# Optimization experiments

Hardware: AMD Instinct MI355X
Metric: run time of the kernel (lower is better)

Reference implementation:

```python
import jax, jax.numpy as jnp
import numpy as np

B, N, H = 4, 4096, 64
T1 = 3072  # num_types = [0, 3072, 1024]


def _xavier(key, shape):
    fan_in, fan_out = shape[1], shape[0]
    lim = float(np.sqrt(6.0 / (fan_in + fan_out)))
    return jax.random.uniform(key, shape, jnp.float32, -lim, lim)


def setup_inputs() -> dict:
    key = jax.random.key(0)
    ks = jax.random.split(key, 16)
    adjacency = (jax.random.uniform(ks[0], (N, N)) < 0.05).astype(jnp.float32)
    adjacency = jnp.maximum(adjacency, jnp.eye(N, dtype=jnp.float32))  # avoid all-zero rows
    return {
        "hidden_states": jax.random.normal(ks[1], (B, N, H), jnp.float32),
        "input_states": jax.random.normal(ks[2], (B, 1, 1), jnp.float32),
        "adjacency": adjacency,
        "Wq": _xavier(ks[3], (H, H)),
        "Wk": _xavier(ks[4], (H, H)),
        "Wv": _xavier(ks[5], (H, H)),
        "Wu_inter": _xavier(ks[6], (H, H)),
        "bu_inter": jnp.zeros((H,), jnp.float32),
        "Wt_inter": _xavier(ks[7], (H, H)),
        "bt_inter": jnp.zeros((H,), jnp.float32),
        "Wu_out": _xavier(ks[8], (H, H)),
        "bu_out": jnp.zeros((H,), jnp.float32),
        "Wt_out": _xavier(ks[9], (H, H)),
        "bt_out": jnp.zeros((H,), jnp.float32),
        "step_size": jnp.float32(0.01),
    }


def reference(hidden_states, input_states, adjacency, Wq, Wk, Wv,
              Wu_inter, bu_inter, Wt_inter, bt_inter,
              Wu_out, bu_out, Wt_out, bt_out, step_size):
    # AccumulatorFunction: adjacency-masked QK^T, L2-norm rows (NOT softmax), aggregate V
    mask = adjacency.T  # [N, N]
    q = hidden_states @ Wq.T  # [B, N, H]
    k = hidden_states @ Wk.T
    v = hidden_states @ Wv.T
    rel = jnp.einsum('bnd,bmd->bnm', q, k) * mask  # [B, N, N]
    rel = rel / jnp.linalg.norm(rel, axis=2, keepdims=True)
    acc = jnp.einsum('bnm,bmd->bnd', rel, v)  # [B, N, H]

    # update_hidden_states with num_types = [0, T1, N - T1]
    def branch(h, a, Wu, bu, Wt, bt):
        dt = 2.0 * jax.nn.sigmoid(h @ Wt.T + bt) - 1.0
        return h + step_size * dt * (a @ Wu.T + bu)

    upd_inter = branch(hidden_states[:, :T1], acc[:, :T1],
                       Wu_inter, bu_inter, Wt_inter, bt_inter)
    upd_out = branch(hidden_states[:, T1:], acc[:, T1:],
                     Wu_out, bu_out, Wt_out, bt_out)
    return jnp.concatenate([upd_inter, upd_out], axis=1)  # [B, N, H]
```

## Files before the change

### kernel.cpp

```cpp
#include <hip/hip_runtime.h>
#include <hip/hip_bf16.h>
#include <math.h>

#define Bb 4
#define Nn 4096
#define Hh 64
#define T1c 3072
#define MC 4

typedef unsigned short ushort_t;
typedef __bf16 bf16x8 __attribute__((ext_vector_type(8)));
typedef float floatx4 __attribute__((ext_vector_type(4)));
typedef float floatx16 __attribute__((ext_vector_type(16)));
typedef unsigned short ushort4v __attribute__((ext_vector_type(4)));

__device__ ushort_t g_qw[(size_t)Bb * Nn * Hh];
__device__ ushort_t g_kw[(size_t)Bb * Nn * Hh];
__device__ ushort_t g_vt[(size_t)Bb * Nn * Hh];
__device__ ushort_t g_dt[(size_t)Bb * Nn * Hh];
__device__ float    g_pac[(size_t)Bb * 64 * MC * 64 * 64];
__device__ float    g_pss[(size_t)Bb * 64 * MC * 64];

__device__ __forceinline__ float bf2f(unsigned short u) {
    union { unsigned int i; float f; } c;
    c.i = ((unsigned int)u) << 16;
    return c.f;
}
__device__ __forceinline__ unsigned short f2bf(float f) {
    union { float f; unsigned int i; } c;
    c.f = f;
    unsigned int x = c.i;
    unsigned int r = (x + 0x7fffu + ((x >> 16) & 1u)) >> 16;
    return (unsigned short)r;
}

__device__ __forceinline__ bf16x8 ld8(const void* p, size_t eidx, bool f32) {
    if (f32) {
        const float* fp = (const float*)p + eidx;
        float4 x0 = *(const float4*)fp;
        float4 x1 = *(const float4*)(fp + 4);
        bf16x8 r;
        r[0] = (__bf16)x0.x; r[1] = (__bf16)x0.y; r[2] = (__bf16)x0.z; r[3] = (__bf16)x0.w;
        r[4] = (__bf16)x1.x; r[5] = (__bf16)x1.y; r[6] = (__bf16)x1.z; r[7] = (__bf16)x1.w;
        return r;
    }
    return *(const bf16x8*)((const ushort_t*)p + eidx);
}
__device__ __forceinline__ float ldS(const void* p, size_t eidx, bool f32) {
    return f32 ? ((const float*)p)[eidx] : bf2f(((const ushort_t*)p)[eidx]);
}
__device__ __forceinline__ void stOut(void* p, size_t eidx, float v, bool f32) {
    if (f32) ((float*)p)[eidx] = v;
    else ((ushort_t*)p)[eidx] = f2bf(v);
}

__device__ __forceinline__ floatx4 mfma16(bf16x8 a, bf16x8 b, floatx4 c) {
    return __builtin_amdgcn_mfma_f32_16x16x32_bf16(a, b, c, 0, 0, 0);
}
__device__ __forceinline__ floatx16 mfma32(bf16x8 a, bf16x8 b, floatx16 c) {
    return __builtin_amdgcn_mfma_f32_32x32x16_bf16(a, b, c, 0, 0, 0);
}

__device__ __forceinline__ float fast_tanh(float x) {
    float e = __expf(-2.0f * fabsf(x));
    float t = (1.0f - e) / (1.0f + e);
    return copysignf(t, x);
}

__global__ __launch_bounds__(256) void qkvt_kernel(
    const void* __restrict__ hid, const void* __restrict__ adj,
    const void* __restrict__ Wq, const void* __restrict__ Wk,
    const void* __restrict__ Wv,
    const void* __restrict__ Wti, const void* __restrict__ bti,
    const void* __restrict__ Wto, const void* __restrict__ bto)
{
    const bool F32 = (*(const unsigned*)adj) == 0x3F800000u;

    const int bi = blockIdx.x;
    const int b = bi >> 8;
    const int n16 = (bi & 255) << 4;
    const int t = threadIdx.x;
    const int wv = t >> 6, lane = t & 63, l16 = lane & 15, quad = lane >> 4;
    const bool inter = (n16 < T1c);

    const void* W = (wv == 0) ? Wq : (wv == 1) ? Wk : (wv == 2) ? Wv
                    : (inter ? Wti : Wto);
    const void* bt = inter ? bti : bto;

    const size_t hbase = ((size_t)(b * Nn + n16 + l16)) * Hh + quad * 8;
    bf16x8 a0 = ld8(hid, hbase, F32);
    bf16x8 a1 = ld8(hid, hbase + 32, F32);
    floatx4 z = {0.f, 0.f, 0.f, 0.f};

    floatx4 c[4];
#pragma unroll
    for (int ti = 0; ti < 4; ++ti) {
        const size_t wrow = (size_t)(ti * 16 + l16) * 64 + quad * 8;
        bf16x8 w0 = ld8(W, wrow, F32);
        bf16x8 w1 = ld8(W, wrow + 32, F32);
        c[ti] = mfma16(a1, w1, mfma16(a0, w0, z));
    }

    if (wv == 0 || wv == 1) {
        ushort_t* dst = (wv == 0) ? g_qw : g_kw;
#pragma unroll
        for (int ti = 0; ti < 4; ++ti)
#pragma unroll
            for (int r = 0; r < 4; ++r)
                dst[((size_t)(b * Nn + n16 + quad * 4 + r)) * 64 + ti * 16 + l16] = f2bf(c[ti][r]);
    } else if (wv == 2) {
#pragma unroll
        for (int ti = 0; ti < 4; ++ti) {
            uint2 pk;
            pk.x = (unsigned)f2bf(c[ti][0]) | ((unsigned)f2bf(c[ti][1]) << 16);
            pk.y = (unsigned)f2bf(c[ti][2]) | ((unsigned)f2bf(c[ti][3]) << 16);
            *(uint2*)&g_vt[((size_t)(b * 64 + ti * 16 + l16)) * Nn + n16 + quad * 4] = pk;
        }
    } else {
#pragma unroll
        for (int ti = 0; ti < 4; ++ti) {
            const float btv = ldS(bt, ti * 16 + l16, F32);
#pragma unroll
            for (int r = 0; r < 4; ++r)
                g_dt[((size_t)(b * Nn + n16 + quad * 4 + r)) * 64 + ti * 16 + l16] =
                    f2bf(fast_tanh(0.5f * (c[ti][r] + btv)));
        }
    }
}

__global__ __launch_bounds__(256, 4) void attn_part_kernel(
    const void* __restrict__ adj)
{
    const bool F32 = (*(const unsigned*)adj) == 0x3F800000u;

    __shared__ __align__(16) ushort_t kT[64 * 72];
    __shared__ __align__(16) ushort_t vTl[64 * 72];
    __shared__ __align__(16) ushort_t sS[64 * 72];
    __shared__ __align__(4)  unsigned char bmB[64 * 8];
    __shared__ float ssqArr[4 * 64];

    const int bi = blockIdx.x;
    const int b  = bi >> 8;
    const int mc = bi & 3;
    const int nt = (bi >> 2) & 63;
    const int n0 = nt << 6;
    const int t = threadIdx.x;
    const int wv = t >> 6, lane = t & 63;
    const int l32 = lane & 31, h = lane >> 5;
    const int nh = wv >> 1, mh = wv & 1;

    bf16x8 qf[4];
#pragma unroll
    for (int i = 0; i < 4; ++i)
        qf[i] = *(const bf16x8*)&g_qw[((size_t)(b * Nn + n0 + nh * 32 + l32)) * 64 + h * 8 + 16 * i];

    floatx16 acc;
    float ssq[16];
#pragma unroll
    for (int r = 0; r < 16; ++r) { acc[r] = 0.f; ssq[r] = 0.f; }

    int srow[2], scol[2];
#pragma unroll
    for (int i = 0; i < 2; ++i) { const int cc = t + 256 * i; srow[i] = cc >> 3; scol[i] = (cc & 7) * 8; }

    for (int it = 0; it < 1024 / 64; ++it) {
        const int m0 = mc * 1024 + it * 64;

#pragma unroll
        for (int i = 0; i < 2; ++i) {
            *(bf16x8*)&kT[srow[i] * 72 + scol[i]] =
                *(const bf16x8*)&g_kw[((size_t)(b * Nn + m0 + srow[i])) * 64 + scol[i]];
            *(bf16x8*)&vTl[srow[i] * 72 + scol[i]] =
                *(const bf16x8*)&g_vt[((size_t)(b * 64 + srow[i])) * Nn + m0 + scol[i]];
            unsigned byte = 0;
            if (F32) {
                const float* fp = (const float*)adj + (size_t)(m0 + srow[i]) * Nn + n0 + scol[i];
                float4 x0 = *(const float4*)fp;
                float4 x1 = *(const float4*)(fp + 4);
                byte = (unsigned)(x0.x != 0.f)        | ((unsigned)(x0.y != 0.f) << 1)
                     | ((unsigned)(x0.z != 0.f) << 2) | ((unsigned)(x0.w != 0.f) << 3)
                     | ((unsigned)(x1.x != 0.f) << 4) | ((unsigned)(x1.y != 0.f) << 5)
                     | ((unsigned)(x1.z != 0.f) << 6) | ((unsigned)(x1.w != 0.f) << 7);
            } else {
                const ushort_t* up = (const ushort_t*)adj + (size_t)(m0 + srow[i]) * Nn + n0 + scol[i];
#pragma unroll
                for (int j = 0; j < 8; ++j) byte |= (unsigned)(up[j] != 0) << j;
            }
            bmB[srow[i] * 8 + (scol[i] >> 3)] = (unsigned char)byte;
        }
        __syncthreads();

        floatx16 s;
#pragma unroll
        for (int r = 0; r < 16; ++r) s[r] = 0.f;
#pragma unroll
        for (int i = 0; i < 4; ++i) {
            bf16x8 kf = *(const bf16x8*)&kT[(mh * 32 + l32) * 72 + h * 8 + 16 * i];
            s = mfma32(qf[i], kf, s);
        }
        const unsigned mw = *(const unsigned*)&bmB[(mh * 32 + l32) * 8 + nh * 4];
        __bf16* sSb = (__bf16*)sS;
#pragma unroll
        for (int r = 0; r < 16; ++r) {
            const int rp = (r & 3) + 8 * (r >> 2) + 4 * h;
            const float sm = ((mw >> rp) & 1u) ? s[r] : 0.f;
            ssq[r] += sm * sm;
            sSb[(nh * 32 + rp) * 72 + mh * 32 + l32] = (__bf16)sm;
        }
        __syncthreads();

#pragma unroll
        for (int i = 0; i < 4; ++i) {
            bf16x8 sf = *(const bf16x8*)&sS[(nh * 32 + l32) * 72 + h * 8 + 16 * i];
            bf16x8 vf = *(const bf16x8*)&vTl[(mh * 32 + l32) * 72 + h * 8 + 16 * i];
            acc = mfma32(sf, vf, acc);
        }
        __syncthreads();
    }

    const size_t pbase = ((size_t)(b * 64 + nt) * MC + mc);

#pragma unroll
    for (int r = 0; r < 16; ++r) {
        float v = ssq[r];
        v += __shfl_xor(v, 1, 64);
        v += __shfl_xor(v, 2, 64);
        v += __shfl_xor(v, 4, 64);
        v += __shfl_xor(v, 8, 64);
        v += __shfl_xor(v, 16, 64);
        ssq[r] = v;
    }
    if (l32 == 0) {
#pragma unroll
        for (int r = 0; r < 16; ++r) {
            const int rp = (r & 3) + 8 * (r >> 2) + 4 * h;
            ssqArr[wv * 64 + nh * 32 + rp] = ssq[r];
        }
    }
    __syncthreads();
    if (t < 64) {
        const int w0 = (t >> 5) * 2;
        g_pss[pbase * 64 + t] = ssqArr[w0 * 64 + t] + ssqArr[(w0 + 1) * 64 + t];
    }

#pragma unroll
    for (int r = 0; r < 16; ++r) {
        const int n = nh * 32 + (r & 3) + 8 * (r >> 2) + 4 * h;
        g_pac[(pbase * 64 + n) * 64 + mh * 32 + l32] = acc[r];
    }
}

__global__ __launch_bounds__(256) void finish_kernel(
    const void* __restrict__ hid, const void* __restrict__ adj,
    const void* __restrict__ Wui, const void* __restrict__ bui,
    const void* __restrict__ Wuo, const void* __restrict__ buo,
    const void* __restrict__ stepp, void* __restrict__ outp)
{
    const bool F32 = (*(const unsigned*)adj) == 0x3F800000u;

    const int bi = blockIdx.x;
    const int b = bi >> 8;
    const int r16 = bi & 255;
    const int n16 = r16 << 4;
    const int nt = r16 >> 2;
    const int nloc0 = (r16 & 3) << 4;
    const int t = threadIdx.x;
    const int wv = t >> 6, lane = t & 63, l16 = lane & 15, quad = lane >> 4;

    const size_t sbase = ((size_t)(b * 64 + nt) * MC + quad) * 64 + nloc0 + l16;
    float sv = g_pss[sbase];
    sv += __shfl_xor(sv, 16, 64);
    sv += __shfl_xor(sv, 32, 64);
    const float inv = (sv > 0.f) ? __frsqrt_rn(sv) : 0.f;

    float s0[8], s1[8];
#pragma unroll
    for (int j = 0; j < 8; ++j) { s0[j] = 0.f; s1[j] = 0.f; }
#pragma unroll
    for (int mcq = 0; mcq < MC; ++mcq) {
        const size_t abase =
            (((size_t)(b * 64 + nt) * MC + mcq) * 64 + nloc0 + l16) * 64 + quad * 8;
        float4 x0 = *(const float4*)&g_pac[abase];
        float4 x1 = *(const float4*)&g_pac[abase + 4];
        float4 y0 = *(const float4*)&g_pac[abase + 32];
        float4 y1 = *(const float4*)&g_pac[abase + 36];
        s0[0] += x0.x; s0[1] += x0.y; s0[2] += x0.z; s0[3] += x0.w;
        s0[4] += x1.x; s0[5] += x1.y; s0[6] += x1.z; s0[7] += x1.w;
        s1[0] += y0.x; s1[1] += y0.y; s1[2] += y0.z; s1[3] += y0.w;
        s1[4] += y1.x; s1[5] += y1.y; s1[6] += y1.z; s1[7] += y1.w;
    }
    bf16x8 ua0, ua1;
#pragma unroll
    for (int j = 0; j < 8; ++j) {
        ua0[j] = (__bf16)(s0[j] * inv);
        ua1[j] = (__bf16)(s1[j] * inv);
    }

    const bool inter = (n16 < T1c);
    const void* Wu = inter ? Wui : Wuo;
    const void* bu = inter ? bui : buo;
    const float step = ldS(stepp, 0, F32);

    const int ti = wv;
    floatx4 z = {0.f, 0.f, 0.f, 0.f};
    const size_t wrow = (size_t)(ti * 16 + l16) * 64 + quad * 8;
    bf16x8 w0 = ld8(Wu, wrow, F32);
    bf16x8 w1 = ld8(Wu, wrow + 32, F32);
    floatx4 u = mfma16(ua1, w1, mfma16(ua0, w0, z));
    const float buv = ldS(bu, ti * 16 + l16, F32);
#pragma unroll
    for (int r = 0; r < 4; ++r) {
        const size_t idx = ((size_t)(b * Nn + n16 + quad * 4 + r)) * 64 + ti * 16 + l16;
        const float hv = ldS(hid, idx, F32);
        const float dtv = bf2f(g_dt[idx]);
        stOut(outp, idx, hv + step * dtv * (u[r] + buv), F32);
    }
}

extern "C" void kernel_launch(void* const* d_in, const int* in_sizes, int n_in,
                              void* d_out, int out_size, void* d_ws, size_t ws_size,
                              hipStream_t stream)
{
    const void* hid = d_in[0];
    const void* adj = d_in[2];
    const void* Wq  = d_in[3];
    const void* Wk  = d_in[4];
    const void* Wv  = d_in[5];
    const void* Wui = d_in[6];
    const void* bui = d_in[7];
    const void* Wti = d_in[8];
    const void* bti = d_in[9];
    const void* Wuo = d_in[10];
    const void* buo = d_in[11];
    const void* Wto = d_in[12];
    const void* bto = d_in[13];
    const void* stepp = d_in[14];

    qkvt_kernel<<<dim3(Bb * (Nn / 16)), dim3(256), 0, stream>>>(
        hid, adj, Wq, Wk, Wv, Wti, bti, Wto, bto);
    attn_part_kernel<<<dim3(Bb * 64 * MC), dim3(256), 0, stream>>>(adj);
    finish_kernel<<<dim3(Bb * (Nn / 16)), dim3(256), 0, stream>>>(
        hid, adj, Wui, bui, Wuo, buo, stepp, d_out);
}
```

Before: 182.3 us.

## Precompute adjacency bitmask once and keep scores in registers for PV MFMA

Adds a bm_kernel that packs the adjacency matrix into a transposed 64-bit ballot bitmask once, instead of each batch's attention blocks re-reading and packing the full fp32 adjacency. In the attention kernel, QK^T is computed transposed so the masked score fragment can feed the PV MFMA directly from registers. This removes the shared-memory score buffer and one barrier per iteration. Each wave now accumulates both 32-column halves of V, and the mh halves are reduced through shared memory at the end. The cost is an extra kernel launch plus a strided per-element adjacency read in bm_kernel, and more accumulator registers per wave.

```diff
diff --git a/kernel.cpp b/kernel.cpp
--- a/kernel.cpp
+++ b/kernel.cpp
@@ -9,15 +9,16 @@
 #define MC 4
 
 typedef unsigned short ushort_t;
+typedef __bf16 bf16x4 __attribute__((ext_vector_type(4)));
 typedef __bf16 bf16x8 __attribute__((ext_vector_type(8)));
 typedef float floatx4 __attribute__((ext_vector_type(4)));
 typedef float floatx16 __attribute__((ext_vector_type(16)));
-typedef unsigned short ushort4v __attribute__((ext_vector_type(4)));
 
 __device__ ushort_t g_qw[(size_t)Bb * Nn * Hh];
 __device__ ushort_t g_kw[(size_t)Bb * Nn * Hh];
 __device__ ushort_t g_vt[(size_t)Bb * Nn * Hh];
 __device__ ushort_t g_dt[(size_t)Bb * Nn * Hh];
+__device__ unsigned long long g_bm[(size_t)Nn * (Nn / 64)];
 __device__ float    g_pac[(size_t)Bb * 64 * MC * 64 * 64];
 __device__ float    g_pss[(size_t)Bb * 64 * MC * 64];
 
@@ -60,6 +61,12 @@
 __device__ __forceinline__ floatx16 mfma32(bf16x8 a, bf16x8 b, floatx16 c) {
     return __builtin_amdgcn_mfma_f32_32x32x16_bf16(a, b, c, 0, 0, 0);
 }
+__device__ __forceinline__ bf16x8 cat44(bf16x4 lo, bf16x4 hi) {
+    bf16x8 r;
+    r[0] = lo[0]; r[1] = lo[1]; r[2] = lo[2]; r[3] = lo[3];
+    r[4] = hi[0]; r[5] = hi[1]; r[6] = hi[2]; r[7] = hi[3];
+    return r;
+}
 
 __device__ __forceinline__ float fast_tanh(float x) {
     float e = __expf(-2.0f * fabsf(x));
@@ -128,16 +135,31 @@
     }
 }
 
-__global__ __launch_bounds__(256, 4) void attn_part_kernel(
-    const void* __restrict__ adj)
+__global__ __launch_bounds__(256) void bm_kernel(const void* __restrict__ adj)
 {
     const bool F32 = (*(const unsigned*)adj) == 0x3F800000u;
-
-    __shared__ __align__(16) ushort_t kT[64 * 72];
-    __shared__ __align__(16) ushort_t vTl[64 * 72];
-    __shared__ __align__(16) ushort_t sS[64 * 72];
-    __shared__ __align__(4)  unsigned char bmB[64 * 8];
-    __shared__ float ssqArr[4 * 64];
+    const int bi = blockIdx.x;
+    const int mt = bi & 63;
+    const int nc = bi >> 6;
+    const int w = threadIdx.x >> 6, lane = threadIdx.x & 63;
+    const int n0 = nc * 256 + w * 64;
+    const size_t rowoff = (size_t)(mt * 64 + lane) * Nn;
+
+    for (int j = 0; j < 64; ++j) {
+        const int n = n0 + j;
+        const float v = ldS(adj, rowoff + n, F32);
+        const unsigned long long m = __ballot(v != 0.f);
+        if (lane == 0) g_bm[(size_t)n * 64 + mt] = m;
+    }
+}
+
+__global__ __launch_bounds__(256, 4) void attn_part_kernel()
+{
+    __shared__ __align__(16) unsigned char smem[64 * 72 * 2 * 2 + 256];
+    ushort_t* kT  = (ushort_t*)smem;
+    ushort_t* vTl = kT + 64 * 72;
+
+    const unsigned* bm32 = (const unsigned*)g_bm;
 
     const int bi = blockIdx.x;
     const int b  = bi >> 8;
@@ -154,16 +176,18 @@
     for (int i = 0; i < 4; ++i)
         qf[i] = *(const bf16x8*)&g_qw[((size_t)(b * Nn + n0 + nh * 32 + l32)) * 64 + h * 8 + 16 * i];
 
-    floatx16 acc;
-    float ssq[16];
-#pragma unroll
-    for (int r = 0; r < 16; ++r) { acc[r] = 0.f; ssq[r] = 0.f; }
+    floatx16 acc[2];
+#pragma unroll
+    for (int dt = 0; dt < 2; ++dt)
+#pragma unroll
+        for (int r = 0; r < 16; ++r) acc[dt][r] = 0.f;
+    float ssql = 0.f;
 
     int srow[2], scol[2];
 #pragma unroll
     for (int i = 0; i < 2; ++i) { const int cc = t + 256 * i; srow[i] = cc >> 3; scol[i] = (cc & 7) * 8; }
 
-    for (int it = 0; it < 1024 / 64; ++it) {
+    for (int it = 0; it < 16; ++it) {
         const int m0 = mc * 1024 + it * 64;
 
 #pragma unroll
@@ -172,21 +196,6 @@
                 *(const bf16x8*)&g_kw[((size_t)(b * Nn + m0 + srow[i])) * 64 + scol[i]];
             *(bf16x8*)&vTl[srow[i] * 72 + scol[i]] =
                 *(const bf16x8*)&g_vt[((size_t)(b * 64 + srow[i])) * Nn + m0 + scol[i]];
-            unsigned byte = 0;
-            if (F32) {
-                const float* fp = (const float*)adj + (size_t)(m0 + srow[i]) * Nn + n0 + scol[i];
-                float4 x0 = *(const float4*)fp;
-                float4 x1 = *(const float4*)(fp + 4);
-                byte = (unsigned)(x0.x != 0.f)        | ((unsigned)(x0.y != 0.f) << 1)
-                     | ((unsigned)(x0.z != 0.f) << 2) | ((unsigned)(x0.w != 0.f) << 3)
-                     | ((unsigned)(x1.x != 0.f) << 4) | ((unsigned)(x1.y != 0.f) << 5)
-                     | ((unsigned)(x1.z != 0.f) << 6) | ((unsigned)(x1.w != 0.f) << 7);
-            } else {
-                const ushort_t* up = (const ushort_t*)adj + (size_t)(m0 + srow[i]) * Nn + n0 + scol[i];
-#pragma unroll
-                for (int j = 0; j < 8; ++j) byte |= (unsigned)(up[j] != 0) << j;
-            }
-            bmB[srow[i] * 8 + (scol[i] >> 3)] = (unsigned char)byte;
         }
         __syncthreads();
 
@@ -196,57 +205,59 @@
 #pragma unroll
         for (int i = 0; i < 4; ++i) {
             bf16x8 kf = *(const bf16x8*)&kT[(mh * 32 + l32) * 72 + h * 8 + 16 * i];
-            s = mfma32(qf[i], kf, s);
-        }
-        const unsigned mw = *(const unsigned*)&bmB[(mh * 32 + l32) * 8 + nh * 4];
-        __bf16* sSb = (__bf16*)sS;
+            s = mfma32(kf, qf[i], s);
+        }
+
+        const unsigned mw = bm32[(size_t)(n0 + nh * 32 + l32) * 128 + mc * 32 + it * 2 + mh];
+        bf16x8 af0, af1;
 #pragma unroll
         for (int r = 0; r < 16; ++r) {
             const int rp = (r & 3) + 8 * (r >> 2) + 4 * h;
             const float sm = ((mw >> rp) & 1u) ? s[r] : 0.f;
-            ssq[r] += sm * sm;
-            sSb[(nh * 32 + rp) * 72 + mh * 32 + l32] = (__bf16)sm;
+            ssql += sm * sm;
+            if (r < 8) af0[r] = (__bf16)sm; else af1[r - 8] = (__bf16)sm;
+        }
+
+#pragma unroll
+        for (int dt = 0; dt < 2; ++dt) {
+            const int vrow = (dt * 32 + l32) * 72 + mh * 32 + 4 * h;
+            bf16x4 lo0 = *(const bf16x4*)&vTl[vrow];
+            bf16x4 hi0 = *(const bf16x4*)&vTl[vrow + 8];
+            acc[dt] = mfma32(af0, cat44(lo0, hi0), acc[dt]);
+            bf16x4 lo1 = *(const bf16x4*)&vTl[vrow + 16];
+            bf16x4 hi1 = *(const bf16x4*)&vTl[vrow + 16 + 8];
+            acc[dt] = mfma32(af1, cat44(lo1, hi1), acc[dt]);
         }
         __syncthreads();
-
-#pragma unroll
-        for (int i = 0; i < 4; ++i) {
-            bf16x8 sf = *(const bf16x8*)&sS[(nh * 32 + l32) * 72 + h * 8 + 16 * i];
-            bf16x8 vf = *(const bf16x8*)&vTl[(mh * 32 + l32) * 72 + h * 8 + 16 * i];
-            acc = mfma32(sf, vf, acc);
-        }
-        __syncthreads();
-    }
-
-    const size_t pbase = ((size_t)(b * 64 + nt) * MC + mc);
-
-#pragma unroll
-    for (int r = 0; r < 16; ++r) {
-        float v = ssq[r];
-        v += __shfl_xor(v, 1, 64);
-        v += __shfl_xor(v, 2, 64);
-        v += __shfl_xor(v, 4, 64);
-        v += __shfl_xor(v, 8, 64);
-        v += __shfl_xor(v, 16, 64);
-        ssq[r] = v;
-    }
-    if (l32 == 0) {
-#pragma unroll
-        for (int r = 0; r < 16; ++r) {
-            const int rp = (r & 3) + 8 * (r >> 2) + 4 * h;
-            ssqArr[wv * 64 + nh * 32 + rp] = ssq[r];
-        }
+    }
+
+    ssql += __shfl_xor(ssql, 32, 64);
+
+    float* accbuf = (float*)smem;
+    float* ssqbuf = (float*)(smem + 16384);
+    if (mh == 1) {
+#pragma unroll
+        for (int dt = 0; dt < 2; ++dt)
+#pragma unroll
+            for (int r = 0; r < 16; ++r) {
+                const int rp = (r & 3) + 8 * (r >> 2) + 4 * h;
+                accbuf[((size_t)nh * 32 + rp) * 64 + dt * 32 + l32] = acc[dt][r];
+            }
+        if (h == 0) ssqbuf[nh * 32 + l32] = ssql;
     }
     __syncthreads();
-    if (t < 64) {
-        const int w0 = (t >> 5) * 2;
-        g_pss[pbase * 64 + t] = ssqArr[w0 * 64 + t] + ssqArr[(w0 + 1) * 64 + t];
-    }
-
-#pragma unroll
-    for (int r = 0; r < 16; ++r) {
-        const int n = nh * 32 + (r & 3) + 8 * (r >> 2) + 4 * h;
-        g_pac[(pbase * 64 + n) * 64 + mh * 32 + l32] = acc[r];
+    if (mh == 0) {
+        const size_t pbase = ((size_t)(b * 64 + nt) * MC + mc);
+#pragma unroll
+        for (int dt = 0; dt < 2; ++dt)
+#pragma unroll
+            for (int r = 0; r < 16; ++r) {
+                const int rp = (r & 3) + 8 * (r >> 2) + 4 * h;
+                const float v = acc[dt][r] + accbuf[((size_t)nh * 32 + rp) * 64 + dt * 32 + l32];
+                g_pac[(pbase * 64 + nh * 32 + rp) * 64 + dt * 32 + l32] = v;
+            }
+        ssql += ssqbuf[nh * 32 + l32];
+        if (h == 0) g_pss[pbase * 64 + nh * 32 + l32] = ssql;
     }
 }
 
@@ -338,7 +349,8 @@
 
     qkvt_kernel<<<dim3(Bb * (Nn / 16)), dim3(256), 0, stream>>>(
         hid, adj, Wq, Wk, Wv, Wti, bti, Wto, bto);
-    attn_part_kernel<<<dim3(Bb * 64 * MC), dim3(256), 0, stream>>>(adj);
+    bm_kernel<<<dim3(1024), dim3(256), 0, stream>>>(adj);
+    attn_part_kernel<<<dim3(Bb * 64 * MC), dim3(256), 0, stream>>>();
     finish_kernel<<<dim3(Bb * (Nn / 16)), dim3(256), 0, stream>>>(
         hid, adj, Wui, bui, Wuo, buo, stepp, d_out);
 }
```

Measured after the change: 246.7 us. +35.4%, slower.
